# Kernel optimization log

Measured on AMD Instinct MI355X. Metric: run time of the kernel, lower is better.

## Reference

```python
import jax, jax.numpy as jnp
import numpy as np


def _chamfer(src, tgt):
    # src: [B, N, 3], tgt: [B, M, 3]
    x2 = jnp.sum(src * src, axis=-1)              # [B, N]
    y2 = jnp.sum(tgt * tgt, axis=-1)              # [B, M]
    xy = jnp.einsum('bnd,bmd->bnm', src, tgt)     # [B, N, M]
    d2 = x2[:, :, None] + y2[:, None, :] - 2.0 * xy
    d2 = jnp.maximum(d2, 0.0)                     # guard tiny negatives
    cham_x = jnp.min(d2, axis=2)                  # [B, N] min over tgt
    cham_y = jnp.min(d2, axis=1)                  # [B, M] min over src
    # point_reduction='mean', batch_reduction='sum'
    loss = jnp.sum(jnp.mean(cham_x, axis=1)) + jnp.sum(jnp.mean(cham_y, axis=1))
    return loss


def setup_inputs() -> dict:
    key = jax.random.key(0)
    k1, k2 = jax.random.split(key)
    src = jax.random.normal(k1, (16, 4096, 3), dtype=jnp.float32)
    tgt = jax.random.normal(k2, (16, 4096, 3), dtype=jnp.float32)
    return {"src": src, "tgt": tgt}


def reference(src, tgt):
    wgeo = 1.0
    return wgeo * _chamfer(src, tgt)
```

## Files before the change

kernel.cpp:

```cpp
#include <hip/hip_runtime.h>
#include <hip/hip_bf16.h>


#define BATCH   16
#define NPTS    4096
#define NSTRIPS 32
#define NH      2
#define COLS_PB 2048
#define CHUNKC  512
#define NCHUNKS (COLS_PB / CHUNKC)
#define NSTEP   (CHUNKC / 64)

typedef __attribute__((ext_vector_type(8)))  short short8;
typedef __attribute__((ext_vector_type(16))) float float16;

union U4S8 { uint4 u; short8 s; };

__device__ inline unsigned int bfb(float v) {
    __hip_bfloat16 h = __float2bfloat16(v);
    unsigned short u; __builtin_memcpy(&u, &h, 2);
    return (unsigned int)u;
}
__device__ inline float bff(float v) { return __bfloat162float(__float2bfloat16(v)); }

#define ONEB 0x3F80u

__device__ inline void buildA(float x, float y, float z, uint4& w0, uint4& w1) {
    float xhf = bff(x), yhf = bff(y), zhf = bff(z);
    float f = fmaf(x, x, fmaf(y, y, z * z));
    float fhf = bff(f);
    unsigned xh = bfb(xhf), yh = bfb(yhf), zh = bfb(zhf);
    unsigned xl = bfb(x - xhf), yl = bfb(y - yhf), zl = bfb(z - zhf);
    unsigned fh = bfb(fhf), fl = bfb(f - fhf);
    w0 = make_uint4(xh | (yh << 16), zh | (xh << 16),
                    yh | (zh << 16), xl | (yl << 16));
    w1 = make_uint4(zl | (fh << 16), fl | (ONEB << 16), ONEB, 0u);
}

__device__ inline void buildB(float x, float y, float z, uint4& w0, uint4& w1) {
    float xhf = bff(x), yhf = bff(y), zhf = bff(z);
    float f = fmaf(x, x, fmaf(y, y, z * z));
    float fhf = bff(f);
    unsigned a = bfb(-2.0f * xhf), b = bfb(-2.0f * yhf), c = bfb(-2.0f * zhf);
    unsigned d = bfb(-2.0f * (x - xhf)), e = bfb(-2.0f * (y - yhf)),
             g = bfb(-2.0f * (z - zhf));
    unsigned fh = bfb(fhf), fl = bfb(f - fhf);
    w0 = make_uint4(a | (b << 16), c | (d << 16),
                    e | (g << 16), a | (b << 16));
    w1 = make_uint4(c | (ONEB << 16), ONEB | (fh << 16), fl, 0u);
}

__device__ inline float tree16(const float16& a) {
    float m0 = fminf(fminf(a[0],  a[1]),  a[2]);
    float m1 = fminf(fminf(a[3],  a[4]),  a[5]);
    float m2 = fminf(fminf(a[6],  a[7]),  a[8]);
    float m3 = fminf(fminf(a[9],  a[10]), a[11]);
    float m4 = fminf(fminf(a[12], a[13]), a[14]);
    float p0 = fminf(fminf(m0, m1), a[15]);
    float p1 = fminf(fminf(m2, m3), m4);
    return fminf(p0, p1);
}

__global__ __launch_bounds__(256, 4) void chamfer_main(
    const float* __restrict__ src, const float* __restrict__ tgt,
    unsigned* __restrict__ wsC, unsigned* __restrict__ wsR)
{
    __shared__ uint4 sbuf[2][2][CHUNKC];
    __shared__ unsigned colpart[COLS_PB];

    int blk = blockIdx.x;
    const int strip = blk & (NSTRIPS - 1); blk >>= 5;
    const int b     = blk & 15;            blk >>= 4;
    const int q     = blk;
    const int qoff  = q * COLS_PB;

    const int t    = threadIdx.x;
    const int lane = t & 63;
    const int w    = t >> 6;
    const int h    = lane >> 5;
    const int l5   = lane & 31;

    const float* Araw = src + (size_t)b * NPTS * 3;
    const float* Braw = tgt + (size_t)b * NPTS * 3;

    short8 afr;
    {
        int row = strip * 128 + w * 32 + l5;
        uint4 w0, w1;
        buildA(Araw[3 * row], Araw[3 * row + 1], Araw[3 * row + 2], w0, w1);
        U4S8 tt; tt.u = h ? w1 : w0;
        afr = tt.s;
    }

#pragma unroll
    for (int i = 0; i < COLS_PB / 256; i++) colpart[t + i * 256] = 0xFFFFFFFFu;

    float nx[2][3];
    auto loadRaw = [&](int c) {
#pragma unroll
        for (int k = 0; k < 2; k++) {
            int p = qoff + c * CHUNKC + t + k * 256;
            nx[k][0] = Braw[3 * p + 0];
            nx[k][1] = Braw[3 * p + 1];
            nx[k][2] = Braw[3 * p + 2];
        }
    };
    auto convertWrite = [&](int bi) {
#pragma unroll
        for (int k = 0; k < 2; k++) {
            int lp = t + k * 256;
            uint4 w0, w1;
            buildB(nx[k][0], nx[k][1], nx[k][2], w0, w1);
            sbuf[bi][0][lp] = w0;
            sbuf[bi][1][lp] = w1;
        }
    };

    const float16 z16 = {0.f,0.f,0.f,0.f,0.f,0.f,0.f,0.f,
                         0.f,0.f,0.f,0.f,0.f,0.f,0.f,0.f};
    float rm[16];
#pragma unroll
    for (int r = 0; r < 16; r++) rm[r] = 1e30f;

    loadRaw(0);
    convertWrite(0);
    for (int c = 0; c < NCHUNKS; c++) {
        __syncthreads();
        if (c + 1 < NCHUNKS) loadRaw(c + 1);
        const int bi = c & 1;

        U4S8 c0, c1, n0, n1;
        c0.u = sbuf[bi][h][l5];
        c1.u = sbuf[bi][h][32 + l5];
#pragma unroll 4
        for (int j2 = 0; j2 < NSTEP; j2++) {
            int nj = (j2 + 1) & (NSTEP - 1);
            n0.u = sbuf[bi][h][nj * 64 + l5];
            n1.u = sbuf[bi][h][nj * 64 + 32 + l5];
            float16 a0 = __builtin_amdgcn_mfma_f32_32x32x16_bf16(afr, c0.s, z16, 0, 0, 0);
            float16 a1 = __builtin_amdgcn_mfma_f32_32x32x16_bf16(afr, c1.s, z16, 0, 0, 0);
#pragma unroll
            for (int r = 0; r < 16; r++)
                rm[r] = fminf(fminf(a0[r], a1[r]), rm[r]);
            float cm0 = tree16(a0);
            float cm1 = tree16(a1);
            const int col = c * CHUNKC + j2 * 64 + l5;
            atomicMin(&colpart[col],      __float_as_uint(fmaxf(cm0, 0.0f)));
            atomicMin(&colpart[col + 32], __float_as_uint(fmaxf(cm1, 0.0f)));
            c0 = n0; c1 = n1;
        }
        if (c + 1 < NCHUNKS) convertWrite((c + 1) & 1);
    }

    __syncthreads();
#pragma unroll
    for (int i = 0; i < COLS_PB / 256; i++) {
        const int idx = t + i * 256;
        atomicMin(&wsC[(size_t)b * NPTS + qoff + idx], colpart[idx]);
    }

#pragma unroll
    for (int mask = 1; mask <= 16; mask <<= 1)
#pragma unroll
        for (int r = 0; r < 16; r++)
            rm[r] = fminf(rm[r], __shfl_xor(rm[r], mask, 64));

    __syncthreads();
    if (l5 == 0) {
#pragma unroll
        for (int r = 0; r < 16; r++) {
            const int row = w * 32 + (r & 3) + 8 * (r >> 2) + 4 * h;
            colpart[row] = __float_as_uint(fmaxf(rm[r], 0.0f));
        }
    }
    __syncthreads();
    if (t < 128)
        atomicMin(&wsR[(size_t)b * NPTS + strip * 128 + t], colpart[t]);
}

__global__ __launch_bounds__(256) void finish_reduce(
    const unsigned* __restrict__ wsC, const unsigned* __restrict__ wsR,
    float* __restrict__ out)
{
    __shared__ float wsum[4];
    const int b = blockIdx.x;
    float v = 0.0f;
#pragma unroll
    for (int i = 0; i < 16; i++)
        v += __uint_as_float(wsC[(size_t)b * NPTS + threadIdx.x + i * 256]);
#pragma unroll
    for (int i = 0; i < 16; i++)
        v += __uint_as_float(wsR[(size_t)b * NPTS + threadIdx.x + i * 256]);
#pragma unroll
    for (int mask = 1; mask <= 32; mask <<= 1) v += __shfl_xor(v, mask, 64);
    if ((threadIdx.x & 63) == 0) wsum[threadIdx.x >> 6] = v;
    __syncthreads();
    if (threadIdx.x == 0)
        atomicAdd(out, (wsum[0] + wsum[1] + wsum[2] + wsum[3]) * (1.0f / (float)NPTS));
}

extern "C" void kernel_launch(void* const* d_in, const int* in_sizes, int n_in,
                              void* d_out, int out_size, void* d_ws, size_t ws_size,
                              hipStream_t stream)
{
    const float* src = (const float*)d_in[0];
    const float* tgt = (const float*)d_in[1];
    float* out = (float*)d_out;
    unsigned* wsC = (unsigned*)d_ws;
    unsigned* wsR = wsC + (size_t)BATCH * NPTS;

    hipMemsetAsync(out, 0, sizeof(float), stream);
    hipMemsetAsync(d_ws, 0xFF, (size_t)2 * BATCH * NPTS * sizeof(unsigned), stream);
    chamfer_main <<<NH * BATCH * NSTRIPS, 256, 0, stream>>>(src, tgt, wsC, wsR);
    finish_reduce<<<BATCH, 256, 0, stream>>>(wsC, wsR, out);
}
```

Baseline: 78.67 us.

## Split column-min LDS per half-wave, single-buffer B, LDS row reduce, single-block finish

Gives each half of the wave its own column-min array in shared memory, which halves atomicMin contention, and merges the two halves before the global atomic. The B staging buffer becomes single-buffered, so each chunk now needs an extra barrier plus an inline convert/write, trading overlap for less LDS. The row-min reduction switches from 80 cross-lane shuffles to an XOR-swizzled LDS transpose. The finish kernel becomes one 1024-thread block that writes the output directly, which drops the output memset and the float atomicAdd.

```diff
diff --git a/kernel.cpp b/kernel.cpp
--- a/kernel.cpp
+++ b/kernel.cpp
@@ -5,7 +5,7 @@
 #define BATCH   16
 #define NPTS    4096
 #define NSTRIPS 32
-#define NH      2
+#define NQ      2
 #define COLS_PB 2048
 #define CHUNKC  512
 #define NCHUNKS (COLS_PB / CHUNKC)
@@ -65,8 +65,8 @@
     const float* __restrict__ src, const float* __restrict__ tgt,
     unsigned* __restrict__ wsC, unsigned* __restrict__ wsR)
 {
-    __shared__ uint4 sbuf[2][2][CHUNKC];
-    __shared__ unsigned colpart[COLS_PB];
+    __shared__ uint4     sbuf[2][CHUNKC];
+    __shared__ unsigned  colpart2[2][COLS_PB];
 
     int blk = blockIdx.x;
     const int strip = blk & (NSTRIPS - 1); blk >>= 5;
@@ -92,8 +92,13 @@
         afr = tt.s;
     }
 
-#pragma unroll
-    for (int i = 0; i < COLS_PB / 256; i++) colpart[t + i * 256] = 0xFFFFFFFFu;
+    {
+        uint4* cp = (uint4*)&colpart2[0][0];
+#pragma unroll
+        for (int i = 0; i < 4; i++)
+            cp[t + i * 256] = make_uint4(0xFFFFFFFFu, 0xFFFFFFFFu,
+                                         0xFFFFFFFFu, 0xFFFFFFFFu);
+    }
 
     float nx[2][3];
     auto loadRaw = [&](int c) {
@@ -105,14 +110,14 @@
             nx[k][2] = Braw[3 * p + 2];
         }
     };
-    auto convertWrite = [&](int bi) {
+    auto convertWrite = [&]() {
 #pragma unroll
         for (int k = 0; k < 2; k++) {
             int lp = t + k * 256;
             uint4 w0, w1;
             buildB(nx[k][0], nx[k][1], nx[k][2], w0, w1);
-            sbuf[bi][0][lp] = w0;
-            sbuf[bi][1][lp] = w1;
+            sbuf[0][lp] = w0;
+            sbuf[1][lp] = w1;
         }
     };
 
@@ -123,20 +128,20 @@
     for (int r = 0; r < 16; r++) rm[r] = 1e30f;
 
     loadRaw(0);
-    convertWrite(0);
     for (int c = 0; c < NCHUNKS; c++) {
+        if (c) __syncthreads();
+        convertWrite();
         __syncthreads();
         if (c + 1 < NCHUNKS) loadRaw(c + 1);
-        const int bi = c & 1;
 
         U4S8 c0, c1, n0, n1;
-        c0.u = sbuf[bi][h][l5];
-        c1.u = sbuf[bi][h][32 + l5];
+        c0.u = sbuf[h][l5];
+        c1.u = sbuf[h][32 + l5];
 #pragma unroll 4
-        for (int j2 = 0; j2 < NSTEP; j2++) {
-            int nj = (j2 + 1) & (NSTEP - 1);
-            n0.u = sbuf[bi][h][nj * 64 + l5];
-            n1.u = sbuf[bi][h][nj * 64 + 32 + l5];
+        for (int j = 0; j < NSTEP; j++) {
+            int nj = (j + 1) & (NSTEP - 1);
+            n0.u = sbuf[h][nj * 64 + l5];
+            n1.u = sbuf[h][nj * 64 + 32 + l5];
             float16 a0 = __builtin_amdgcn_mfma_f32_32x32x16_bf16(afr, c0.s, z16, 0, 0, 0);
             float16 a1 = __builtin_amdgcn_mfma_f32_32x32x16_bf16(afr, c1.s, z16, 0, 0, 0);
 #pragma unroll
@@ -144,59 +149,59 @@
                 rm[r] = fminf(fminf(a0[r], a1[r]), rm[r]);
             float cm0 = tree16(a0);
             float cm1 = tree16(a1);
-            const int col = c * CHUNKC + j2 * 64 + l5;
-            atomicMin(&colpart[col],      __float_as_uint(fmaxf(cm0, 0.0f)));
-            atomicMin(&colpart[col + 32], __float_as_uint(fmaxf(cm1, 0.0f)));
+            const int col = c * CHUNKC + j * 64 + l5;
+            atomicMin(&colpart2[h][col],      __float_as_uint(fmaxf(cm0, 0.0f)));
+            atomicMin(&colpart2[h][col + 32], __float_as_uint(fmaxf(cm1, 0.0f)));
             c0 = n0; c1 = n1;
         }
-        if (c + 1 < NCHUNKS) convertWrite((c + 1) & 1);
-    }
-
-    __syncthreads();
+    }
+    __syncthreads();
+
 #pragma unroll
     for (int i = 0; i < COLS_PB / 256; i++) {
-        const int idx = t + i * 256;
-        atomicMin(&wsC[(size_t)b * NPTS + qoff + idx], colpart[idx]);
-    }
-
-#pragma unroll
-    for (int mask = 1; mask <= 16; mask <<= 1)
-#pragma unroll
-        for (int r = 0; r < 16; r++)
-            rm[r] = fminf(rm[r], __shfl_xor(rm[r], mask, 64));
-
-    __syncthreads();
-    if (l5 == 0) {
-#pragma unroll
-        for (int r = 0; r < 16; r++) {
-            const int row = w * 32 + (r & 3) + 8 * (r >> 2) + 4 * h;
-            colpart[row] = __float_as_uint(fmaxf(rm[r], 0.0f));
-        }
-    }
-    __syncthreads();
-    if (t < 128)
-        atomicMin(&wsR[(size_t)b * NPTS + strip * 128 + t], colpart[t]);
-}
-
-__global__ __launch_bounds__(256) void finish_reduce(
-    const unsigned* __restrict__ wsC, const unsigned* __restrict__ wsR,
-    float* __restrict__ out)
+        const int col = t + i * 256;
+        unsigned v = min(colpart2[0][col], colpart2[1][col]);
+        atomicMin(&wsC[(size_t)b * NPTS + qoff + col], v);
+    }
+    __syncthreads();
+
+    float* rowbuf = (float*)&colpart2[0][0];
+#pragma unroll
+    for (int r = 0; r < 16; r++) {
+        const int rl = (r & 3) + 8 * (r >> 2) + 4 * h;
+        rowbuf[(w * 32 + rl) * 32 + (l5 ^ rl)] = rm[r];
+    }
+    __syncthreads();
+    if (t < 128) {
+        const int rl = t & 31;
+        float m = 1e30f;
+#pragma unroll
+        for (int cc = 0; cc < 32; cc++)
+            m = fminf(m, rowbuf[t * 32 + (cc ^ rl)]);
+        atomicMin(&wsR[(size_t)b * NPTS + strip * 128 + t],
+                  __float_as_uint(fmaxf(m, 0.0f)));
+    }
+}
+
+__global__ __launch_bounds__(1024) void finish_reduce(
+    const unsigned* __restrict__ ws, float* __restrict__ out)
 {
-    __shared__ float wsum[4];
-    const int b = blockIdx.x;
+    __shared__ float wsum[16];
+    const int t = threadIdx.x;
     float v = 0.0f;
 #pragma unroll
-    for (int i = 0; i < 16; i++)
-        v += __uint_as_float(wsC[(size_t)b * NPTS + threadIdx.x + i * 256]);
-#pragma unroll
-    for (int i = 0; i < 16; i++)
-        v += __uint_as_float(wsR[(size_t)b * NPTS + threadIdx.x + i * 256]);
+    for (int i = 0; i < 2 * BATCH * NPTS / 1024; i++)
+        v += __uint_as_float(ws[t + i * 1024]);
 #pragma unroll
     for (int mask = 1; mask <= 32; mask <<= 1) v += __shfl_xor(v, mask, 64);
-    if ((threadIdx.x & 63) == 0) wsum[threadIdx.x >> 6] = v;
-    __syncthreads();
-    if (threadIdx.x == 0)
-        atomicAdd(out, (wsum[0] + wsum[1] + wsum[2] + wsum[3]) * (1.0f / (float)NPTS));
+    if ((t & 63) == 0) wsum[t >> 6] = v;
+    __syncthreads();
+    if (t < 64) {
+        float s = (t < 16) ? wsum[t] : 0.0f;
+#pragma unroll
+        for (int mask = 1; mask <= 8; mask <<= 1) s += __shfl_xor(s, mask, 64);
+        if (t == 0) out[0] = s * (1.0f / (float)NPTS);
+    }
 }
 
 extern "C" void kernel_launch(void* const* d_in, const int* in_sizes, int n_in,
@@ -209,8 +214,7 @@
     unsigned* wsC = (unsigned*)d_ws;
     unsigned* wsR = wsC + (size_t)BATCH * NPTS;
 
-    hipMemsetAsync(out, 0, sizeof(float), stream);
     hipMemsetAsync(d_ws, 0xFF, (size_t)2 * BATCH * NPTS * sizeof(unsigned), stream);
-    chamfer_main <<<NH * BATCH * NSTRIPS, 256, 0, stream>>>(src, tgt, wsC, wsR);
-    finish_reduce<<<BATCH, 256, 0, stream>>>(wsC, wsR, out);
-}
+    chamfer_main <<<NQ * BATCH * NSTRIPS, 256, 0, stream>>>(src, tgt, wsC, wsR);
+    finish_reduce<<<1, 1024, 0, stream>>>(wsC, out);
+}
```

Measured after the change: 106.3 us. 1.35x slower.
